# Optimization experiments

Hardware: AMD Instinct MI355X
Metric: run time of the kernel (lower is better)

Reference implementation:

```python
import jax, jax.numpy as jnp
import numpy as np

FORGET_BIAS = 1.0  # TF BasicLSTMCell default


def setup_inputs() -> dict:
    key = jax.random.key(0)
    ks = jax.random.split(key, 6)
    B, T, D, H, A = 32, 2048, 256, 256, 18
    x = jax.random.normal(ks[0], (B, T, D), dtype=jnp.float32)
    seq_lens = jax.random.randint(ks[1], (B,), 1, T + 1, dtype=jnp.int32)
    c_in = jnp.zeros((B, H), dtype=jnp.float32)
    h_in = jnp.zeros((B, H), dtype=jnp.float32)
    W = jax.random.normal(ks[2], (D + H, 4 * H), dtype=jnp.float32) * 0.05
    b = jnp.zeros((4 * H,), dtype=jnp.float32)
    W_out = jax.random.normal(ks[3], (H, A), dtype=jnp.float32) * 0.01
    b_out = jnp.zeros((A,), dtype=jnp.float32)
    return {"x": x, "seq_lens": seq_lens, "c_in": c_in, "h_in": h_in,
            "W": W, "b": b, "W_out": W_out, "b_out": b_out}


def _lstm_scan(x, seq_lens, c_in, h_in, W, b):
    B, T, D = x.shape
    H = c_in.shape[-1]
    xs = jnp.swapaxes(x, 0, 1)  # [T, B, D] time-major for scan
    ts = jnp.arange(T, dtype=jnp.int32)

    def step(carry, inp):
        c, h = carry
        xt, t = inp
        gates = jnp.concatenate([xt, h], axis=-1) @ W + b  # [B, 4H]
        i, j, f, o = jnp.split(gates, 4, axis=-1)  # TF gate order i, j, f, o
        new_c = c * jax.nn.sigmoid(f + FORGET_BIAS) + jax.nn.sigmoid(i) * jnp.tanh(j)
        new_h = jnp.tanh(new_c) * jax.nn.sigmoid(o)
        mask = (t < seq_lens)[:, None]  # [B, 1]; dynamic_rnn semantics
        c = jnp.where(mask, new_c, c)
        h = jnp.where(mask, new_h, h)
        out = jnp.where(mask, new_h, jnp.zeros_like(new_h))  # zero past length
        return (c, h), out

    (c_fin, h_fin), ys = jax.lax.scan(step, (c_in, h_in), (xs, ts))
    return jnp.swapaxes(ys, 0, 1), c_fin, h_fin  # ys: [B, T, H]


def reference(x, seq_lens, c_in, h_in, W, b, W_out, b_out):
    lstm_out, c_fin, h_fin = _lstm_scan(x, seq_lens, c_in, h_in, W, b)
    H = c_in.shape[-1]
    last_layer = lstm_out.reshape(-1, H)  # [B*T, H]
    logits = last_layer @ W_out + b_out   # [B*T, A]
    return logits, last_layer, c_fin, h_fin
```

## Files before the change

kernel.cpp:

```cpp
#include <hip/hip_runtime.h>
#include <hip/hip_bf16.h>

typedef __attribute__((ext_vector_type(2))) _Float16 half2v;
typedef __attribute__((ext_vector_type(4))) float f32x4;

__device__ __forceinline__ unsigned short f2h_bits(float f) {
    _Float16 h = (_Float16)f;
    return __builtin_bit_cast(unsigned short, h);
}
__device__ __forceinline__ float sigf(float x) { return 1.0f / (1.0f + __expf(-x)); }
__device__ __forceinline__ float tanhf_fast(float x) {
    float ax = fabsf(x);
    float e = __expf(-2.0f * ax);
    float t = (1.0f - e) / (1.0f + e);
    return copysignf(t, x);
}
__device__ __forceinline__ float dot2u(unsigned int w, unsigned int h, float acc) {
    return __builtin_amdgcn_fdot2(__builtin_bit_cast(half2v, w),
                                  __builtin_bit_cast(half2v, h), acc, false);
}
__device__ __forceinline__ float dot2x4(uint4 w, uint4 h, float acc) {
    acc = dot2u(w.x, h.x, acc);
    acc = dot2u(w.y, h.y, acc);
    acc = dot2u(w.z, h.z, acc);
    acc = dot2u(w.w, h.w, acc);
    return acc;
}
__device__ __forceinline__ void pin(uint4& v) {
    asm volatile("" : "+v"(v.x), "+v"(v.y), "+v"(v.z), "+v"(v.w));
}

__global__ void k_flag0(int* __restrict__ prog) { *prog = 0; }

__global__ __launch_bounds__(256) void k_prep(const float* __restrict__ W,
                                              unsigned short* __restrict__ wht) {
    int idx = blockIdx.x * 256 + threadIdx.x;
    int g = idx >> 8, k = idx & 255;
    wht[idx] = f2h_bits(W[(size_t)(256 + k) * 1024 + g]);
}

__global__ __launch_bounds__(256) void k_init(const float* __restrict__ cin,
                                              const float* __restrict__ hin,
                                              float* __restrict__ cc,
                                              float* __restrict__ ch) {
    int i = blockIdx.x * 256 + threadIdx.x;
    cc[i] = cin[i];
    ch[i] = hin[i];
}

__global__ __launch_bounds__(256) void k_gates(const float* __restrict__ x,
                                               const float* __restrict__ W,
                                               const float* __restrict__ bias,
                                               float* __restrict__ gates,
                                               int C, int t0) {
    __shared__ float xs[32][256];
    int tid = threadIdx.x;
    int tc = tid & 31, tr = tid >> 5;
    int r0 = (blockIdx.x >> 3) * 32;
    int c0 = (blockIdx.x & 7) * 128;
    int b  = r0 / C;
    int tl = r0 - b * C;
    const float* xbase = x + ((size_t)b * 2048 + t0 + tl) * 256;

    for (int i = tid; i < 2048; i += 256) {
        int r = i >> 6, kq = (i & 63) << 2;
        *(f32x4*)&xs[r][kq] = *(const f32x4*)(xbase + (size_t)r * 256 + kq);
    }
    __syncthreads();

    f32x4 acc[4];
    f32x4 bb = *(const f32x4*)(bias + c0 + tc * 4);
#pragma unroll
    for (int i = 0; i < 4; ++i) acc[i] = bb;
    const float* wp = W + c0 + tc * 4;
    for (int k = 0; k < 256; k += 2) {
        f32x4 w0 = *(const f32x4*)(wp + (size_t)k * 1024);
        f32x4 w1 = *(const f32x4*)(wp + (size_t)(k + 1) * 1024);
#pragma unroll
        for (int i = 0; i < 4; ++i) {
            float2 xv = *(const float2*)&xs[tr * 4 + i][k];
            acc[i] += w0 * xv.x;
            acc[i] += w1 * xv.y;
        }
    }
#pragma unroll
    for (int i = 0; i < 4; ++i)
        *(f32x4*)(gates + (size_t)(r0 + tr * 4 + i) * 1024 + c0 + tc * 4) = acc[i];
}

__global__ __launch_bounds__(512)
__attribute__((amdgpu_waves_per_eu(2, 2)))
void k_rnn(const unsigned short* __restrict__ wht,
           const float* __restrict__ gates,
           const int* __restrict__ seq_lens,
           float* __restrict__ carry_c,
           float* __restrict__ carry_h,
           int* __restrict__ prog,
           int C, int t0,
           float* __restrict__ out_ll,
           float* __restrict__ out_c,
           float* __restrict__ out_h) {
    extern __shared__ unsigned int smem[];
    uint4* ildsq = (uint4*)smem;
    unsigned short* hs = (unsigned short*)(ildsq + 8192);
    const int tid = threadIdx.x;
    const int u = tid >> 1, p = tid & 1;
    const int w = tid >> 6, l = tid & 63;
    const int b = blockIdx.x;
    if (b == 0 && tid == 0) *prog = 1;

    const uint4* whtq = (const uint4*)wht;
    uint4 wj[16], wf[16], wo[16];
#pragma unroll
    for (int j = 0; j < 16; ++j) {
        wj[j] = whtq[(size_t)(256 + u) * 32 + p * 16 + j];
        wf[j] = whtq[(size_t)(512 + u) * 32 + p * 16 + j];
        wo[j] = whtq[(size_t)(768 + u) * 32 + p * 16 + j];
    }
#pragma unroll
    for (int j = 0; j < 16; ++j) { pin(wj[j]); pin(wf[j]); pin(wo[j]); }
#pragma unroll
    for (int j = 0; j < 16; ++j)
        ildsq[(w * 16 + j) * 64 + l] = whtq[(size_t)u * 32 + p * 16 + j];
    if (b == 0 && tid == 0) *prog = 2;

    float c = carry_c[b * 256 + u];
    float h = carry_h[b * 256 + u];
    if (p == 0) hs[u] = f2h_bits(h);
    int ns = seq_lens[b] - t0;
    ns = ns < 0 ? 0 : (ns > C ? C : ns);
    const float* gxb = gates + (size_t)b * C * 1024;
    float gi = gxb[u], gj = gxb[256 + u], gf = gxb[512 + u], go = gxb[768 + u];
    __syncthreads();

    for (int t = 0; t < ns; ++t) {
        const uint4* hp = (const uint4*)(hs + (t & 1) * 256) + p * 16;
        float ni = 0.f, nj = 0.f, nf = 0.f, no = 0.f;
        if (t + 1 < ns) {
            const float* gn = gxb + (size_t)(t + 1) * 1024;
            ni = gn[u]; nj = gn[256 + u]; nf = gn[512 + u]; no = gn[768 + u];
        }
        float ai = p ? 0.f : gi, aj = p ? 0.f : gj;
        float af = p ? 0.f : gf, ao = p ? 0.f : go;
#pragma unroll
        for (int j = 0; j < 16; ++j) {
            uint4 hv = hp[j];
            uint4 iv = ildsq[(w * 16 + j) * 64 + l];
            ai = dot2x4(iv,    hv, ai);
            aj = dot2x4(wj[j], hv, aj);
            af = dot2x4(wf[j], hv, af);
            ao = dot2x4(wo[j], hv, ao);
        }
        ai += __shfl_xor(ai, 1);
        aj += __shfl_xor(aj, 1);
        af += __shfl_xor(af, 1);
        ao += __shfl_xor(ao, 1);
        if (p == 0) {
            float I = sigf(ai);
            float J = tanhf_fast(aj);
            float F = sigf(af + 1.0f);
            float O = sigf(ao);
            c = c * F + I * J;
            h = tanhf_fast(c) * O;
            out_ll[(size_t)(b * 2048 + t0 + t) * 256 + u] = h;
            hs[((t + 1) & 1) * 256 + u] = f2h_bits(h);
        }
        gi = ni; gj = nj; gf = nf; go = no;
        __syncthreads();
    }
    if (p == 0) {
        carry_c[b * 256 + u] = c;
        carry_h[b * 256 + u] = h;
        out_c[b * 256 + u] = c;
        out_h[b * 256 + u] = h;
    }
    f32x4 z = {0.f, 0.f, 0.f, 0.f};
    f32x4* zp = (f32x4*)(out_ll + (size_t)(b * 2048 + t0 + ns) * 256);
    int cnt = (C - ns) * 64;
    for (int i = tid; i < cnt; i += 512) zp[i] = z;
    if (b == 0 && tid == 0) *prog = 3;
}

__global__ __launch_bounds__(256) void k_logits(const float* __restrict__ ll,
                                                const float* __restrict__ wout,
                                                const float* __restrict__ bout,
                                                float* __restrict__ lg) {
    __shared__ float rows[32][260];
    __shared__ float wo[4608];
    int tid = threadIdx.x;
    size_t r0 = (size_t)blockIdx.x * 32;
    for (int i = tid; i < 4608; i += 256) wo[i] = wout[i];
    const f32x4* src = (const f32x4*)(ll + r0 * 256);
    for (int i = tid; i < 2048; i += 256) {
        int row = i >> 6, c4 = (i & 63) * 4;
        *(f32x4*)&rows[row][c4] = src[i];
    }
    __syncthreads();
    for (int o = tid; o < 576; o += 256) {
        int r = o / 18, a = o - r * 18;
        float acc = bout[a];
#pragma unroll 8
        for (int k = 0; k < 256; ++k)
            acc += rows[r][k] * wo[k * 18 + a];
        lg[(r0 + r) * 18 + a] = acc;
    }
}

__global__ __launch_bounds__(256) void k_diag(const float* __restrict__ gates,
                                              const int* __restrict__ prog,
                                              int wsb, int nsample,
                                              float* __restrict__ logit0) {
    __shared__ float red[256];
    int tid = threadIdx.x;
    float m = 0.f; int bad_nan = 0;
    for (int i = tid; i < nsample; i += 256) {
        float v = gates[i];
        if (v != v) bad_nan = 1;
        m = fmaxf(m, fabsf(v));
    }
    red[tid] = bad_nan ? 3.0e38f : m;
    __syncthreads();
    for (int s = 128; s > 0; s >>= 1) {
        if (tid < s) red[tid] = fmaxf(red[tid], red[tid + s]);
        __syncthreads();
    }
    if (tid == 0) {
        float l = log2f(1.0f + red[0]);
        int R = *prog; R = R < 0 ? 0 : (R > 3 ? 3 : R);
        int G = (int)(l * 0.5f); G = G < 0 ? 0 : (G > 7 ? 7 : G);
        int good = (R == 3) && (l <= 4.0f) && (wsb >= 1);
        if (!good) {
            int code = (R << 5) | (G << 2) | wsb;
            *logit0 = (float)(256 + 2 * code);
        }
    }
}

extern "C" void kernel_launch(void* const* d_in, const int* in_sizes, int n_in,
                              void* d_out, int out_size, void* d_ws, size_t ws_size,
                              hipStream_t stream) {
    const float* x = nullptr; const int* seq = nullptr;
    const float* cin = nullptr, *hin = nullptr, *W = nullptr, *bia = nullptr,
               * Wo = nullptr, *bo = nullptr;
    int n8192 = 0;
    for (int i = 0; i < n_in; ++i) {
        switch (in_sizes[i]) {
            case 16777216: x   = (const float*)d_in[i]; break;
            case 32:       seq = (const int*)d_in[i];   break;
            case 524288:   W   = (const float*)d_in[i]; break;
            case 1024:     bia = (const float*)d_in[i]; break;
            case 4608:     Wo  = (const float*)d_in[i]; break;
            case 18:       bo  = (const float*)d_in[i]; break;
            case 8192:
                if (n8192 == 0) cin = (const float*)d_in[i];
                else if (n8192 == 1) hin = (const float*)d_in[i];
                ++n8192; break;
        }
    }
    if (!x)   x   = (const float*)d_in[0];
    if (!seq) seq = (const int*)d_in[1];
    if (!cin) cin = (const float*)d_in[2];
    if (!hin) hin = (const float*)d_in[3];
    if (!W)   W   = (const float*)d_in[4];
    if (!bia) bia = (const float*)d_in[5];
    if (!Wo)  Wo  = (const float*)d_in[6];
    if (!bo)  bo  = (const float*)d_in[7];

    unsigned short* wht = (unsigned short*)d_ws;
    float* carry_c = (float*)((char*)d_ws + 524288);
    float* carry_h = (float*)((char*)d_ws + 557056);
    int*   prog    = (int*)((char*)d_ws + 589824);
    float* gates   = (float*)((char*)d_ws + 593920);
    const size_t fixed = 593920;

    int wsb;
    if (ws_size < fixed + (size_t)64 * 131072) wsb = 0;
    else if (ws_size < ((size_t)70 << 20))  wsb = 1;
    else if (ws_size < ((size_t)280 << 20)) wsb = 2;
    else wsb = 3;

    int C = 2048;
    while (C > 64 && fixed + (size_t)C * 131072 > ws_size) C >>= 1;
    int NC = 2048 / C;

    float* out = (float*)d_out;
    float* o_logits = out;
    float* o_ll = out + 1179648;
    float* o_c  = out + 17956864;
    float* o_h  = out + 17965056;

    (void)hipFuncSetAttribute(reinterpret_cast<const void*>(&k_rnn),
                              hipFuncAttributeMaxDynamicSharedMemorySize, 132096);

    hipLaunchKernelGGL(k_flag0, dim3(1), dim3(1), 0, stream, prog);
    int nsample = 0;
    if (wsb >= 1) {
        hipLaunchKernelGGL(k_prep, dim3(1024), dim3(256), 0, stream, W, wht);
        hipLaunchKernelGGL(k_init, dim3(32),   dim3(256), 0, stream, cin, hin,
                           carry_c, carry_h);
        for (int ch = 0; ch < NC; ++ch) {
            int t0 = ch * C;
            hipLaunchKernelGGL(k_gates, dim3(8 * C), dim3(256), 0, stream,
                               x, W, bia, gates, C, t0);
            hipLaunchKernelGGL(k_rnn, dim3(32), dim3(512), 132096, stream,
                               wht, gates, seq, carry_c, carry_h, prog, C, t0,
                               o_ll, o_c, o_h);
        }
        nsample = 4096;
    }
    hipLaunchKernelGGL(k_logits, dim3(2048), dim3(256), 0, stream, o_ll, Wo, bo, o_logits);
    hipLaunchKernelGGL(k_diag, dim3(1), dim3(256), 0, stream,
                       gates, prog, wsb, nsample, o_logits);
}
```

Before: 4.710 ms.

## Split recurrent dot across four lanes with two units each and pad h buffer

The recurrent step is remapped so each group of four threads computes two hidden units, each lane covering a quarter of the reduction. Each h vector read from shared memory is then reused across eight dot products instead of four, halving h loads per FMA. The h buffer is padded (288 halves per slot) to avoid LDS bank conflicts when the four lanes read different slices. The cost is an extra shuffle stage in the reduction, and only half the threads run the gate nonlinearities.

```diff
diff --git a/kernel.cpp b/kernel.cpp
--- a/kernel.cpp
+++ b/kernel.cpp
@@ -104,75 +104,111 @@
     uint4* ildsq = (uint4*)smem;
     unsigned short* hs = (unsigned short*)(ildsq + 8192);
     const int tid = threadIdx.x;
-    const int u = tid >> 1, p = tid & 1;
     const int w = tid >> 6, l = tid & 63;
+    const int q = tid & 3;
+    const int g = tid >> 2;
+    const int u0 = g * 2;
     const int b = blockIdx.x;
     if (b == 0 && tid == 0) *prog = 1;
 
     const uint4* whtq = (const uint4*)wht;
-    uint4 wj[16], wf[16], wo[16];
-#pragma unroll
-    for (int j = 0; j < 16; ++j) {
-        wj[j] = whtq[(size_t)(256 + u) * 32 + p * 16 + j];
-        wf[j] = whtq[(size_t)(512 + u) * 32 + p * 16 + j];
-        wo[j] = whtq[(size_t)(768 + u) * 32 + p * 16 + j];
-    }
-#pragma unroll
-    for (int j = 0; j < 16; ++j) { pin(wj[j]); pin(wf[j]); pin(wo[j]); }
-#pragma unroll
-    for (int j = 0; j < 16; ++j)
-        ildsq[(w * 16 + j) * 64 + l] = whtq[(size_t)u * 32 + p * 16 + j];
+    uint4 wj[2][8], wf[2][8], wo[2][8];
+#pragma unroll
+    for (int uu = 0; uu < 2; ++uu)
+#pragma unroll
+        for (int jj = 0; jj < 8; ++jj) {
+            wj[uu][jj] = whtq[(size_t)(256 + u0 + uu) * 32 + q * 8 + jj];
+            wf[uu][jj] = whtq[(size_t)(512 + u0 + uu) * 32 + q * 8 + jj];
+            wo[uu][jj] = whtq[(size_t)(768 + u0 + uu) * 32 + q * 8 + jj];
+        }
+#pragma unroll
+    for (int uu = 0; uu < 2; ++uu)
+#pragma unroll
+        for (int jj = 0; jj < 8; ++jj) { pin(wj[uu][jj]); pin(wf[uu][jj]); pin(wo[uu][jj]); }
+
+#pragma unroll
+    for (int uu = 0; uu < 2; ++uu)
+#pragma unroll
+        for (int jj = 0; jj < 8; ++jj)
+            ildsq[(w * 16 + uu * 8 + jj) * 64 + l] = whtq[(size_t)(u0 + uu) * 32 + q * 8 + jj];
     if (b == 0 && tid == 0) *prog = 2;
 
-    float c = carry_c[b * 256 + u];
-    float h = carry_h[b * 256 + u];
-    if (p == 0) hs[u] = f2h_bits(h);
+    float c = 0.f, h = 0.f;
+    if (q < 2) {
+        int ua = u0 + q;
+        c = carry_c[b * 256 + ua];
+        h = carry_h[b * 256 + ua];
+        hs[((ua >> 3) + (ua >> 6)) * 8 + (ua & 7)] = f2h_bits(h);
+    }
     int ns = seq_lens[b] - t0;
     ns = ns < 0 ? 0 : (ns > C ? C : ns);
     const float* gxb = gates + (size_t)b * C * 1024;
-    float gi = gxb[u], gj = gxb[256 + u], gf = gxb[512 + u], go = gxb[768 + u];
+    float gi = 0.f, gj = 0.f, gf = 0.f, go = 0.f;
+    if (q < 2) {
+        int ua = u0 + q;
+        gi = gxb[ua]; gj = gxb[256 + ua]; gf = gxb[512 + ua]; go = gxb[768 + ua];
+    }
+    const uint4* ivp = ildsq + ((w * 16) * 64 + l);
     __syncthreads();
 
     for (int t = 0; t < ns; ++t) {
-        const uint4* hp = (const uint4*)(hs + (t & 1) * 256) + p * 16;
-        float ni = 0.f, nj = 0.f, nf = 0.f, no = 0.f;
-        if (t + 1 < ns) {
+        const uint4* hq = (const uint4*)(hs + (t & 1) * 288) + q * 9;
+        float ni = 0.f, nj = 0.f, nf = 0.f, no_ = 0.f;
+        if (t + 1 < ns && q < 2) {
             const float* gn = gxb + (size_t)(t + 1) * 1024;
-            ni = gn[u]; nj = gn[256 + u]; nf = gn[512 + u]; no = gn[768 + u];
-        }
-        float ai = p ? 0.f : gi, aj = p ? 0.f : gj;
-        float af = p ? 0.f : gf, ao = p ? 0.f : go;
-#pragma unroll
-        for (int j = 0; j < 16; ++j) {
-            uint4 hv = hp[j];
-            uint4 iv = ildsq[(w * 16 + j) * 64 + l];
-            ai = dot2x4(iv,    hv, ai);
-            aj = dot2x4(wj[j], hv, aj);
-            af = dot2x4(wf[j], hv, af);
-            ao = dot2x4(wo[j], hv, ao);
-        }
-        ai += __shfl_xor(ai, 1);
-        aj += __shfl_xor(aj, 1);
-        af += __shfl_xor(af, 1);
-        ao += __shfl_xor(ao, 1);
-        if (p == 0) {
+            int ua = u0 + q;
+            ni = gn[ua]; nj = gn[256 + ua]; nf = gn[512 + ua]; no_ = gn[768 + ua];
+        }
+        float a00 = (q == 0) ? gi : 0.f, a01 = (q == 0) ? gj : 0.f;
+        float a02 = (q == 0) ? gf : 0.f, a03 = (q == 0) ? go : 0.f;
+        float a10 = (q == 1) ? gi : 0.f, a11 = (q == 1) ? gj : 0.f;
+        float a12 = (q == 1) ? gf : 0.f, a13 = (q == 1) ? go : 0.f;
+#pragma unroll
+        for (int j = 0; j < 8; ++j) {
+            uint4 hv  = hq[j];
+            uint4 iv0 = ivp[j << 6];
+            uint4 iv1 = ivp[(8 + j) << 6];
+            a00 = dot2x4(iv0,      hv, a00);
+            a10 = dot2x4(iv1,      hv, a10);
+            a01 = dot2x4(wj[0][j], hv, a01);
+            a11 = dot2x4(wj[1][j], hv, a11);
+            a02 = dot2x4(wf[0][j], hv, a02);
+            a12 = dot2x4(wf[1][j], hv, a12);
+            a03 = dot2x4(wo[0][j], hv, a03);
+            a13 = dot2x4(wo[1][j], hv, a13);
+        }
+        a00 += __shfl_xor(a00, 1); a00 += __shfl_xor(a00, 2);
+        a01 += __shfl_xor(a01, 1); a01 += __shfl_xor(a01, 2);
+        a02 += __shfl_xor(a02, 1); a02 += __shfl_xor(a02, 2);
+        a03 += __shfl_xor(a03, 1); a03 += __shfl_xor(a03, 2);
+        a10 += __shfl_xor(a10, 1); a10 += __shfl_xor(a10, 2);
+        a11 += __shfl_xor(a11, 1); a11 += __shfl_xor(a11, 2);
+        a12 += __shfl_xor(a12, 1); a12 += __shfl_xor(a12, 2);
+        a13 += __shfl_xor(a13, 1); a13 += __shfl_xor(a13, 2);
+        if (q < 2) {
+            float ai = q ? a10 : a00;
+            float aj = q ? a11 : a01;
+            float af = q ? a12 : a02;
+            float ao = q ? a13 : a03;
             float I = sigf(ai);
             float J = tanhf_fast(aj);
             float F = sigf(af + 1.0f);
             float O = sigf(ao);
             c = c * F + I * J;
             h = tanhf_fast(c) * O;
-            out_ll[(size_t)(b * 2048 + t0 + t) * 256 + u] = h;
-            hs[((t + 1) & 1) * 256 + u] = f2h_bits(h);
-        }
-        gi = ni; gj = nj; gf = nf; go = no;
+            int ua = u0 + q;
+            out_ll[(size_t)(b * 2048 + t0 + t) * 256 + ua] = h;
+            hs[((t + 1) & 1) * 288 + ((ua >> 3) + (ua >> 6)) * 8 + (ua & 7)] = f2h_bits(h);
+        }
+        gi = ni; gj = nj; gf = nf; go = no_;
         __syncthreads();
     }
-    if (p == 0) {
-        carry_c[b * 256 + u] = c;
-        carry_h[b * 256 + u] = h;
-        out_c[b * 256 + u] = c;
-        out_h[b * 256 + u] = h;
+    if (q < 2) {
+        int ua = u0 + q;
+        carry_c[b * 256 + ua] = c;
+        carry_h[b * 256 + ua] = h;
+        out_c[b * 256 + ua] = c;
+        out_h[b * 256 + ua] = h;
     }
     f32x4 z = {0.f, 0.f, 0.f, 0.f};
     f32x4* zp = (f32x4*)(out_ll + (size_t)(b * 2048 + t0 + ns) * 256);
@@ -290,7 +326,7 @@
     float* o_h  = out + 17965056;
 
     (void)hipFuncSetAttribute(reinterpret_cast<const void*>(&k_rnn),
-                              hipFuncAttributeMaxDynamicSharedMemorySize, 132096);
+                              hipFuncAttributeMaxDynamicSharedMemorySize, 132224);
 
     hipLaunchKernelGGL(k_flag0, dim3(1), dim3(1), 0, stream, prog);
     int nsample = 0;
@@ -302,7 +338,7 @@
             int t0 = ch * C;
             hipLaunchKernelGGL(k_gates, dim3(8 * C), dim3(256), 0, stream,
                                x, W, bia, gates, C, t0);
-            hipLaunchKernelGGL(k_rnn, dim3(32), dim3(512), 132096, stream,
+            hipLaunchKernelGGL(k_rnn, dim3(32), dim3(512), 132224, stream,
                                wht, gates, seq, carry_c, carry_h, prog, C, t0,
                                o_ll, o_c, o_h);
         }
```

After: 5.255 ms. 1.12x slower.

## Split each hidden unit's recurrent dot product across four lanes with DPP reduction

Applied to the files above, without the earlier changes.

The recurrent kernel now runs 1024 threads per block, and each hidden unit's reduction over K=256 is split across four lanes instead of two. This halves the register-resident weight slices per thread and doubles the waves available to hide latency. Partial sums are combined with DPP quad permutes instead of a shuffle, and the h buffer in shared memory is padded to reduce bank conflicts on the four-way reads. In exchange, each step needs a heavier block-wide barrier and more gate loads, and three of four lanes sit idle during the activation math.

```diff
diff --git a/kernel.cpp b/kernel.cpp
--- a/kernel.cpp
+++ b/kernel.cpp
@@ -28,6 +28,15 @@
 }
 __device__ __forceinline__ void pin(uint4& v) {
     asm volatile("" : "+v"(v.x), "+v"(v.y), "+v"(v.z), "+v"(v.w));
+}
+__device__ __forceinline__ float quad_allsum(float a) {
+    int y = __builtin_amdgcn_update_dpp(0, __builtin_bit_cast(int, a),
+                                        0xB1 , 0xF, 0xF, true);
+    a += __builtin_bit_cast(float, y);
+    y = __builtin_amdgcn_update_dpp(0, __builtin_bit_cast(int, a),
+                                    0x4E , 0xF, 0xF, true);
+    a += __builtin_bit_cast(float, y);
+    return a;
 }
 
 __global__ void k_flag0(int* __restrict__ prog) { *prog = 0; }
@@ -88,8 +97,8 @@
         *(f32x4*)(gates + (size_t)(r0 + tr * 4 + i) * 1024 + c0 + tc * 4) = acc[i];
 }
 
-__global__ __launch_bounds__(512)
-__attribute__((amdgpu_waves_per_eu(2, 2)))
+__global__ __launch_bounds__(1024)
+__attribute__((amdgpu_waves_per_eu(4, 4)))
 void k_rnn(const unsigned short* __restrict__ wht,
            const float* __restrict__ gates,
            const int* __restrict__ seq_lens,
@@ -104,71 +113,79 @@
     uint4* ildsq = (uint4*)smem;
     unsigned short* hs = (unsigned short*)(ildsq + 8192);
     const int tid = threadIdx.x;
-    const int u = tid >> 1, p = tid & 1;
     const int w = tid >> 6, l = tid & 63;
+    const int q = tid & 3;
+    const int u = tid >> 2;
     const int b = blockIdx.x;
     if (b == 0 && tid == 0) *prog = 1;
 
     const uint4* whtq = (const uint4*)wht;
-    uint4 wj[16], wf[16], wo[16];
-#pragma unroll
-    for (int j = 0; j < 16; ++j) {
-        wj[j] = whtq[(size_t)(256 + u) * 32 + p * 16 + j];
-        wf[j] = whtq[(size_t)(512 + u) * 32 + p * 16 + j];
-        wo[j] = whtq[(size_t)(768 + u) * 32 + p * 16 + j];
-    }
-#pragma unroll
-    for (int j = 0; j < 16; ++j) { pin(wj[j]); pin(wf[j]); pin(wo[j]); }
-#pragma unroll
-    for (int j = 0; j < 16; ++j)
-        ildsq[(w * 16 + j) * 64 + l] = whtq[(size_t)u * 32 + p * 16 + j];
+    uint4 wj[8], wf[8], wo[8];
+#pragma unroll
+    for (int j = 0; j < 8; ++j) {
+        wj[j] = whtq[(size_t)(256 + u) * 32 + q * 8 + j];
+        wf[j] = whtq[(size_t)(512 + u) * 32 + q * 8 + j];
+        wo[j] = whtq[(size_t)(768 + u) * 32 + q * 8 + j];
+    }
+
+#pragma unroll
+    for (int j = 0; j < 8; ++j)
+        ildsq[(w * 8 + j) * 64 + l] = whtq[(size_t)u * 32 + q * 8 + j];
     if (b == 0 && tid == 0) *prog = 2;
 
-    float c = carry_c[b * 256 + u];
-    float h = carry_h[b * 256 + u];
-    if (p == 0) hs[u] = f2h_bits(h);
+    float c = 0.f, h = 0.f;
+    if (q == 0) {
+        c = carry_c[b * 256 + u];
+        h = carry_h[b * 256 + u];
+        hs[((u >> 3) + (u >> 6)) * 8 + (u & 7)] = f2h_bits(h);
+    }
     int ns = seq_lens[b] - t0;
     ns = ns < 0 ? 0 : (ns > C ? C : ns);
     const float* gxb = gates + (size_t)b * C * 1024;
-    float gi = gxb[u], gj = gxb[256 + u], gf = gxb[512 + u], go = gxb[768 + u];
+    const int qo = q * 256 + u;
+    float pg = 0.f;
+    if (ns > 0) pg = gxb[qo];
+    const uint4* ivbase = ildsq + (w * 8) * 64 + l;
     __syncthreads();
 
     for (int t = 0; t < ns; ++t) {
-        const uint4* hp = (const uint4*)(hs + (t & 1) * 256) + p * 16;
-        float ni = 0.f, nj = 0.f, nf = 0.f, no = 0.f;
-        if (t + 1 < ns) {
-            const float* gn = gxb + (size_t)(t + 1) * 1024;
-            ni = gn[u]; nj = gn[256 + u]; nf = gn[512 + u]; no = gn[768 + u];
-        }
-        float ai = p ? 0.f : gi, aj = p ? 0.f : gj;
-        float af = p ? 0.f : gf, ao = p ? 0.f : go;
-#pragma unroll
-        for (int j = 0; j < 16; ++j) {
-            uint4 hv = hp[j];
-            uint4 iv = ildsq[(w * 16 + j) * 64 + l];
-            ai = dot2x4(iv,    hv, ai);
-            aj = dot2x4(wj[j], hv, aj);
-            af = dot2x4(wf[j], hv, af);
-            ao = dot2x4(wo[j], hv, ao);
-        }
-        ai += __shfl_xor(ai, 1);
-        aj += __shfl_xor(aj, 1);
-        af += __shfl_xor(af, 1);
-        ao += __shfl_xor(ao, 1);
-        if (p == 0) {
-            float I = sigf(ai);
-            float J = tanhf_fast(aj);
-            float F = sigf(af + 1.0f);
-            float O = sigf(ao);
+#pragma unroll
+        for (int j = 0; j < 8; ++j) { pin(wj[j]); pin(wf[j]); pin(wo[j]); }
+
+        const uint4* hq = (const uint4*)(hs + (t & 1) * 288) + q * 9;
+        float pgn = 0.f;
+        if (t + 1 < ns) pgn = gxb[(size_t)(t + 1) * 1024 + qo];
+        float a0 = (q == 0) ? pg : 0.f;
+        float a1 = (q == 1) ? pg : 0.f;
+        float a2 = (q == 2) ? pg : 0.f;
+        float a3 = (q == 3) ? pg : 0.f;
+#pragma unroll
+        for (int j = 0; j < 8; ++j) {
+            uint4 hv = hq[j];
+            uint4 iv = ivbase[j << 6];
+            a0 = dot2x4(iv,    hv, a0);
+            a1 = dot2x4(wj[j], hv, a1);
+            a2 = dot2x4(wf[j], hv, a2);
+            a3 = dot2x4(wo[j], hv, a3);
+        }
+        a0 = quad_allsum(a0);
+        a1 = quad_allsum(a1);
+        a2 = quad_allsum(a2);
+        a3 = quad_allsum(a3);
+        if (q == 0) {
+            float I = sigf(a0);
+            float J = tanhf_fast(a1);
+            float F = sigf(a2 + 1.0f);
+            float O = sigf(a3);
             c = c * F + I * J;
             h = tanhf_fast(c) * O;
             out_ll[(size_t)(b * 2048 + t0 + t) * 256 + u] = h;
-            hs[((t + 1) & 1) * 256 + u] = f2h_bits(h);
-        }
-        gi = ni; gj = nj; gf = nf; go = no;
+            hs[((t + 1) & 1) * 288 + ((u >> 3) + (u >> 6)) * 8 + (u & 7)] = f2h_bits(h);
+        }
+        pg = pgn;
         __syncthreads();
     }
-    if (p == 0) {
+    if (q == 0) {
         carry_c[b * 256 + u] = c;
         carry_h[b * 256 + u] = h;
         out_c[b * 256 + u] = c;
@@ -177,7 +194,7 @@
     f32x4 z = {0.f, 0.f, 0.f, 0.f};
     f32x4* zp = (f32x4*)(out_ll + (size_t)(b * 2048 + t0 + ns) * 256);
     int cnt = (C - ns) * 64;
-    for (int i = tid; i < cnt; i += 512) zp[i] = z;
+    for (int i = tid; i < cnt; i += 1024) zp[i] = z;
     if (b == 0 && tid == 0) *prog = 3;
 }
 
@@ -290,7 +307,7 @@
     float* o_h  = out + 17965056;
 
     (void)hipFuncSetAttribute(reinterpret_cast<const void*>(&k_rnn),
-                              hipFuncAttributeMaxDynamicSharedMemorySize, 132096);
+                              hipFuncAttributeMaxDynamicSharedMemorySize, 132224);
 
     hipLaunchKernelGGL(k_flag0, dim3(1), dim3(1), 0, stream, prog);
     int nsample = 0;
@@ -302,7 +319,7 @@
             int t0 = ch * C;
             hipLaunchKernelGGL(k_gates, dim3(8 * C), dim3(256), 0, stream,
                                x, W, bia, gates, C, t0);
-            hipLaunchKernelGGL(k_rnn, dim3(32), dim3(512), 132096, stream,
+            hipLaunchKernelGGL(k_rnn, dim3(32), dim3(1024), 132224, stream,
                                wht, gates, seq, carry_c, carry_h, prog, C, t0,
                                o_ll, o_c, o_h);
         }
```

Result: faster. 4.595 ms (-2.5%).

## Compute recurrent matvec with MFMA 16x16x32 f16 and an LDS preactivation exchange

Applied to the files above, without the earlier changes.

Replaces the per-unit fdot2 recurrent matvec with MFMA instructions. The hidden vector is broadcast as the A operand, so only row 0 of each 16x16 tile is useful. The recurrent weights are re-laid out in a new MFMA fragment order: 6 of 8 k-tiles stay in registers and the rest go in LDS. Each wave computes one gate's half of the columns and writes preactivations to LDS, which adds a second barrier per timestep before 256 threads apply the gate nonlinearities. The intent is to cut the serial per-step instruction count, at the cost of wasted MFMA rows, an extra sync and lower lane utilisation in the elementwise phase.

```diff
diff --git a/kernel.cpp b/kernel.cpp
--- a/kernel.cpp
+++ b/kernel.cpp
@@ -3,6 +3,7 @@
 
 typedef __attribute__((ext_vector_type(2))) _Float16 half2v;
 typedef __attribute__((ext_vector_type(4))) float f32x4;
+typedef __attribute__((ext_vector_type(8))) _Float16 f16x8;
 
 __device__ __forceinline__ unsigned short f2h_bits(float f) {
     _Float16 h = (_Float16)f;
@@ -15,19 +16,10 @@
     float t = (1.0f - e) / (1.0f + e);
     return copysignf(t, x);
 }
-__device__ __forceinline__ float dot2u(unsigned int w, unsigned int h, float acc) {
-    return __builtin_amdgcn_fdot2(__builtin_bit_cast(half2v, w),
-                                  __builtin_bit_cast(half2v, h), acc, false);
-}
-__device__ __forceinline__ float dot2x4(uint4 w, uint4 h, float acc) {
-    acc = dot2u(w.x, h.x, acc);
-    acc = dot2u(w.y, h.y, acc);
-    acc = dot2u(w.z, h.z, acc);
-    acc = dot2u(w.w, h.w, acc);
-    return acc;
-}
-__device__ __forceinline__ void pin(uint4& v) {
-    asm volatile("" : "+v"(v.x), "+v"(v.y), "+v"(v.z), "+v"(v.w));
+__device__ __forceinline__ void pinv(f16x8& v) { asm volatile("" : "+v"(v)); }
+
+__device__ __forceinline__ f32x4 mfma16(f16x8 a, f16x8 b, f32x4 c) {
+    return __builtin_amdgcn_mfma_f32_16x16x32_f16(a, b, c, 0, 0, 0);
 }
 
 __global__ void k_flag0(int* __restrict__ prog) { *prog = 0; }
@@ -35,8 +27,15 @@
 __global__ __launch_bounds__(256) void k_prep(const float* __restrict__ W,
                                               unsigned short* __restrict__ wht) {
     int idx = blockIdx.x * 256 + threadIdx.x;
-    int g = idx >> 8, k = idx & 255;
-    wht[idx] = f2h_bits(W[(size_t)(256 + k) * 1024 + g]);
+    int f = idx >> 9;
+    int l = (idx >> 3) & 63;
+    int i = idx & 7;
+    int g  = f >> 7;
+    int nt = (f >> 3) & 15;
+    int kt = f & 7;
+    int k   = kt * 32 + (l >> 4) * 8 + i;
+    int col = g * 256 + nt * 16 + (l & 15);
+    wht[idx] = f2h_bits(W[(size_t)(256 + k) * 1024 + col]);
 }
 
 __global__ __launch_bounds__(256) void k_init(const float* __restrict__ cin,
@@ -101,78 +100,109 @@
            float* __restrict__ out_c,
            float* __restrict__ out_h) {
     extern __shared__ unsigned int smem[];
-    uint4* ildsq = (uint4*)smem;
-    unsigned short* hs = (unsigned short*)(ildsq + 8192);
+    f16x8* bfr = (f16x8*)smem;
+    float* preact = (float*)(bfr + 8192);
+    unsigned short* hs = (unsigned short*)(preact + 1024);
     const int tid = threadIdx.x;
-    const int u = tid >> 1, p = tid & 1;
     const int w = tid >> 6, l = tid & 63;
+    const int gate = w >> 1;
+    const int nth = (w & 1) * 8;
     const int b = blockIdx.x;
     if (b == 0 && tid == 0) *prog = 1;
 
-    const uint4* whtq = (const uint4*)wht;
-    uint4 wj[16], wf[16], wo[16];
-#pragma unroll
-    for (int j = 0; j < 16; ++j) {
-        wj[j] = whtq[(size_t)(256 + u) * 32 + p * 16 + j];
-        wf[j] = whtq[(size_t)(512 + u) * 32 + p * 16 + j];
-        wo[j] = whtq[(size_t)(768 + u) * 32 + p * 16 + j];
-    }
-#pragma unroll
-    for (int j = 0; j < 16; ++j) { pin(wj[j]); pin(wf[j]); pin(wo[j]); }
-#pragma unroll
-    for (int j = 0; j < 16; ++j)
-        ildsq[(w * 16 + j) * 64 + l] = whtq[(size_t)u * 32 + p * 16 + j];
+    const f16x8* whtf = (const f16x8*)wht;
+    f16x8 B[8][6];
+#pragma unroll
+    for (int nt = 0; nt < 8; ++nt)
+#pragma unroll
+        for (int kt = 0; kt < 6; ++kt)
+            B[nt][kt] = whtf[(size_t)(((gate * 16 + nth + nt) * 8 + kt) * 64 + l)];
+#pragma unroll
+    for (int nt = 0; nt < 8; ++nt)
+#pragma unroll
+        for (int kx = 0; kx < 2; ++kx)
+            bfr[((w * 8 + nt) * 2 + kx) * 64 + l] =
+                whtf[(size_t)(((gate * 16 + nth + nt) * 8 + 6 + kx) * 64 + l)];
     if (b == 0 && tid == 0) *prog = 2;
 
-    float c = carry_c[b * 256 + u];
-    float h = carry_h[b * 256 + u];
-    if (p == 0) hs[u] = f2h_bits(h);
+    float c = 0.f, h = 0.f;
+    float pg0 = 0.f, pg1 = 0.f, pg2 = 0.f, pg3 = 0.f;
     int ns = seq_lens[b] - t0;
     ns = ns < 0 ? 0 : (ns > C ? C : ns);
     const float* gxb = gates + (size_t)b * C * 1024;
-    float gi = gxb[u], gj = gxb[256 + u], gf = gxb[512 + u], go = gxb[768 + u];
+    if (tid < 256) {
+        c = carry_c[b * 256 + tid];
+        h = carry_h[b * 256 + tid];
+        hs[tid] = f2h_bits(h);
+        if (ns > 0) {
+            pg0 = gxb[tid];       pg1 = gxb[256 + tid];
+            pg2 = gxb[512 + tid]; pg3 = gxb[768 + tid];
+        }
+    }
     __syncthreads();
 
     for (int t = 0; t < ns; ++t) {
-        const uint4* hp = (const uint4*)(hs + (t & 1) * 256) + p * 16;
-        float ni = 0.f, nj = 0.f, nf = 0.f, no = 0.f;
-        if (t + 1 < ns) {
+#pragma unroll
+        for (int nt = 0; nt < 8; ++nt)
+#pragma unroll
+            for (int kt = 0; kt < 6; ++kt) pinv(B[nt][kt]);
+
+        float ng0 = 0.f, ng1 = 0.f, ng2 = 0.f, ng3 = 0.f;
+        if (t + 1 < ns && tid < 256) {
             const float* gn = gxb + (size_t)(t + 1) * 1024;
-            ni = gn[u]; nj = gn[256 + u]; nf = gn[512 + u]; no = gn[768 + u];
-        }
-        float ai = p ? 0.f : gi, aj = p ? 0.f : gj;
-        float af = p ? 0.f : gf, ao = p ? 0.f : go;
-#pragma unroll
-        for (int j = 0; j < 16; ++j) {
-            uint4 hv = hp[j];
-            uint4 iv = ildsq[(w * 16 + j) * 64 + l];
-            ai = dot2x4(iv,    hv, ai);
-            aj = dot2x4(wj[j], hv, aj);
-            af = dot2x4(wf[j], hv, af);
-            ao = dot2x4(wo[j], hv, ao);
-        }
-        ai += __shfl_xor(ai, 1);
-        aj += __shfl_xor(aj, 1);
-        af += __shfl_xor(af, 1);
-        ao += __shfl_xor(ao, 1);
-        if (p == 0) {
+            ng0 = gn[tid];       ng1 = gn[256 + tid];
+            ng2 = gn[512 + tid]; ng3 = gn[768 + tid];
+        }
+
+        const unsigned short* hb = hs + (t & 1) * 256;
+#pragma unroll
+        for (int p = 0; p < 2; ++p) {
+            f32x4 acc[4];
+            f32x4 z4 = {0.f, 0.f, 0.f, 0.f};
+#pragma unroll
+            for (int j = 0; j < 4; ++j) acc[j] = z4;
+#pragma unroll
+            for (int kt = 0; kt < 8; ++kt) {
+                f16x8 av = *(const f16x8*)(hb + kt * 32 + ((l >> 4) * 8));
+#pragma unroll
+                for (int j = 0; j < 4; ++j) {
+                    const int nt = p * 4 + j;
+                    f16x8 bv;
+                    if (kt < 6) bv = B[nt][kt];
+                    else        bv = bfr[((w * 8 + nt) * 2 + (kt - 6)) * 64 + l];
+                    acc[j] = mfma16(av, bv, acc[j]);
+                }
+            }
+            if (l < 16) {
+#pragma unroll
+                for (int j = 0; j < 4; ++j)
+                    preact[gate * 256 + (nth + p * 4 + j) * 16 + l] = acc[j].x;
+            }
+        }
+        __syncthreads();
+
+        if (tid < 256) {
+            float ai = preact[tid]       + pg0;
+            float aj = preact[256 + tid] + pg1;
+            float af = preact[512 + tid] + pg2;
+            float ao = preact[768 + tid] + pg3;
             float I = sigf(ai);
             float J = tanhf_fast(aj);
             float F = sigf(af + 1.0f);
             float O = sigf(ao);
             c = c * F + I * J;
             h = tanhf_fast(c) * O;
-            out_ll[(size_t)(b * 2048 + t0 + t) * 256 + u] = h;
-            hs[((t + 1) & 1) * 256 + u] = f2h_bits(h);
-        }
-        gi = ni; gj = nj; gf = nf; go = no;
+            out_ll[(size_t)(b * 2048 + t0 + t) * 256 + tid] = h;
+            hs[((t + 1) & 1) * 256 + tid] = f2h_bits(h);
+        }
+        pg0 = ng0; pg1 = ng1; pg2 = ng2; pg3 = ng3;
         __syncthreads();
     }
-    if (p == 0) {
-        carry_c[b * 256 + u] = c;
-        carry_h[b * 256 + u] = h;
-        out_c[b * 256 + u] = c;
-        out_h[b * 256 + u] = h;
+    if (tid < 256) {
+        carry_c[b * 256 + tid] = c;
+        carry_h[b * 256 + tid] = h;
+        out_c[b * 256 + tid] = c;
+        out_h[b * 256 + tid] = h;
     }
     f32x4 z = {0.f, 0.f, 0.f, 0.f};
     f32x4* zp = (f32x4*)(out_ll + (size_t)(b * 2048 + t0 + ns) * 256);
@@ -290,7 +320,7 @@
     float* o_h  = out + 17965056;
 
     (void)hipFuncSetAttribute(reinterpret_cast<const void*>(&k_rnn),
-                              hipFuncAttributeMaxDynamicSharedMemorySize, 132096);
+                              hipFuncAttributeMaxDynamicSharedMemorySize, 136192);
 
     hipLaunchKernelGGL(k_flag0, dim3(1), dim3(1), 0, stream, prog);
     int nsample = 0;
@@ -302,7 +332,7 @@
             int t0 = ch * C;
             hipLaunchKernelGGL(k_gates, dim3(8 * C), dim3(256), 0, stream,
                                x, W, bia, gates, C, t0);
-            hipLaunchKernelGGL(k_rnn, dim3(32), dim3(512), 132096, stream,
+            hipLaunchKernelGGL(k_rnn, dim3(32), dim3(512), 136192, stream,
                                wht, gates, seq, carry_c, carry_h, prog, C, t0,
                                o_ll, o_c, o_h);
         }
```

Result: slower. 8.642 ms (+83.5%).
